# Optimization experiments

Hardware: AMD Instinct MI355X
Metric: run time of the kernel (lower is better)

## Reference

```python
import jax, jax.numpy as jnp
import numpy as np

EMB = 1024
HEADS = 16
HEAD_DIM = EMB // HEADS
BLOCK = 256
N_GLOBAL = 4
WINDOW = 128
ROPE_BASE = 10000.0


def rotate_half(x):
    # interleaved rotate: (-x2_0, x1_0, -x2_1, x1_1, ...), faithful to source
    x1 = x[..., ::2]
    x2 = x[..., 1::2]
    return jnp.stack((-x2, x1), axis=-1).reshape(x.shape)


def setup_inputs() -> dict:
    key = jax.random.key(0)
    k0, k1, k2 = jax.random.split(key, 3)
    B, S = 2, 2048
    x = jax.random.normal(k0, (B, S, EMB), dtype=jnp.float32)
    # Linear weights stored as [in, out]; y = x @ W (bias=False in source)
    w_qkv = jax.random.normal(k1, (EMB, 3 * EMB), dtype=jnp.float32) * (EMB ** -0.5)
    w_out = jax.random.normal(k2, (EMB, EMB), dtype=jnp.float32) * (EMB ** -0.5)
    return {"x": x, "w_qkv": w_qkv, "w_out": w_out}


def _forward(x, w_qkv, w_out):
    B, S, E = x.shape
    H, D = HEADS, HEAD_DIM
    qkv = (x @ w_qkv).reshape(B, S, 3, H, D).transpose(2, 0, 3, 1, 4)  # [3,B,H,S,D]
    q, k, v = qkv[0], qkv[1], qkv[2]

    # Rotary embedding (start_pos = 0, no cache)
    inv_freq = 1.0 / (ROPE_BASE ** (jnp.arange(0, D, 2, dtype=jnp.float32) / D))
    pos = jnp.arange(S, dtype=jnp.float32)
    freqs = jnp.outer(pos, inv_freq)                 # [S, D/2]
    emb = jnp.concatenate([freqs, freqs], axis=-1)   # [S, D]
    cos = jnp.cos(emb)[None, None]                   # [1,1,S,D]
    sin = jnp.sin(emb)[None, None]
    q = q * cos + rotate_half(q) * sin
    k = k * cos + rotate_half(k) * sin

    # Block-local + global-token + sliding-window mask, AND causal (vectorized)
    i = jnp.arange(S)[:, None]
    j = jnp.arange(S)[None, :]
    allowed = (i // BLOCK == j // BLOCK) | (i < N_GLOBAL) | (j < N_GLOBAL) \
              | (jnp.abs(i - j) <= WINDOW)
    allowed = allowed & (j <= i)
    # NOTE: source passes ~mask to F.scaled_dot_product_attention, where a
    # boolean attn_mask with True means "attend". We replicate that exactly.
    attend = ~allowed  # [S, S]

    scale = D ** -0.5
    scores = jnp.einsum("bhsd,bhtd->bhst", q, k) * scale      # [B,H,S,S]
    scores = jnp.where(attend[None, None], scores, jnp.float32(-1e30))
    attn = jax.nn.softmax(scores, axis=-1)
    out = jnp.einsum("bhst,bhtd->bhsd", attn, v)              # [B,H,S,D]
    out = out.transpose(0, 2, 1, 3).reshape(B, S, E)
    return out @ w_out


def reference(x, w_qkv, w_out):
    return _forward(x, w_qkv, w_out)
```

## Files before the change

### kernel.cpp

```cpp
#include <hip/hip_runtime.h>
#include <hip/hip_bf16.h>

#define EMBD   1024
#define NHEAD  16
#define HDIM   64
#define SEQ    2048
#define BATCH  2
#define MROWS  4096
#define NQKV   3072
#define VSTR   2064

using floatx4 = __attribute__((ext_vector_type(4))) float;
using short8  = __attribute__((ext_vector_type(8))) short;

static __device__ __forceinline__ float bf2f(unsigned short u) {
    unsigned int v = ((unsigned int)u) << 16;
    return __uint_as_float(v);
}
static __device__ __forceinline__ unsigned short f2bf(float f) {
    __hip_bfloat16 h = __float2bfloat16(f);
    return *reinterpret_cast<unsigned short*>(&h);
}

__global__ __launch_bounds__(256) void cast_x(
    const float* __restrict__ x, unsigned short* __restrict__ xh,
    unsigned short* __restrict__ xl)
{
    int idx = (blockIdx.x * 256 + threadIdx.x) * 4;
    float4 v = *(const float4*)(x + idx);
    ushort4 h, l;
    h.x = f2bf(v.x); l.x = f2bf(v.x - bf2f(h.x));
    h.y = f2bf(v.y); l.y = f2bf(v.y - bf2f(h.y));
    h.z = f2bf(v.z); l.z = f2bf(v.z - bf2f(h.z));
    h.w = f2bf(v.w); l.w = f2bf(v.w - bf2f(h.w));
    *(ushort4*)(xh + idx) = h;
    *(ushort4*)(xl + idx) = l;
}

__global__ __launch_bounds__(256) void cast_wT(
    const float* __restrict__ w, unsigned short* __restrict__ wT, int N)
{
    __shared__ unsigned short th[64][65];
    const int k0 = blockIdx.y * 64, n0 = blockIdx.x * 64;
    const int t = threadIdx.x;
    const int r = t >> 4, c = (t & 15) * 4;
    for (int rr = r; rr < 64; rr += 16) {
        float4 v = *(const float4*)(w + (size_t)(k0 + rr) * N + n0 + c);
        th[rr][c + 0] = f2bf(v.x);
        th[rr][c + 1] = f2bf(v.y);
        th[rr][c + 2] = f2bf(v.z);
        th[rr][c + 3] = f2bf(v.w);
    }
    __syncthreads();
    for (int rr = r; rr < 64; rr += 16) {
        ushort4 h;
        h.x = th[c + 0][rr]; h.y = th[c + 1][rr];
        h.z = th[c + 2][rr]; h.w = th[c + 3][rr];
        *(ushort4*)(wT + (size_t)(n0 + rr) * 1024 + k0 + c) = h;
    }
}

__global__ __launch_bounds__(256) void gemm_qkv_mfma(
    const unsigned short* __restrict__ xh, const unsigned short* __restrict__ xl,
    const unsigned short* __restrict__ wbT,
    unsigned short* __restrict__ qst, unsigned short* __restrict__ kst,
    unsigned short* __restrict__ vtT)
{
    const int t = threadIdx.x, wave = t >> 6, lane = t & 63;
    const int col = lane & 15, quad = lane >> 4;
    const int n0 = blockIdx.x * 128;
    const int m0 = blockIdx.y * 128;
    const int which = n0 >> 10;
    const int wm = (wave >> 1) * 64, wn = (wave & 1) * 64;

    floatx4 acc[4][4];
    #pragma unroll
    for (int i = 0; i < 4; ++i)
        #pragma unroll
        for (int j = 0; j < 4; ++j) acc[i][j] = (floatx4){0.f, 0.f, 0.f, 0.f};

    const unsigned short* pa_h = xh  + (size_t)(m0 + wm + col) * 1024 + quad * 8;
    const unsigned short* pa_l = xl  + (size_t)(m0 + wm + col) * 1024 + quad * 8;
    const unsigned short* pb   = wbT + (size_t)(n0 + wn + col) * 1024 + quad * 8;

    for (int k0 = 0; k0 < 1024; k0 += 32) {
        short8 bf[4], ah[4], al[4];
        #pragma unroll
        for (int f = 0; f < 4; ++f) bf[f] = *(const short8*)(pb   + f * 16 * 1024 + k0);
        #pragma unroll
        for (int f = 0; f < 4; ++f) ah[f] = *(const short8*)(pa_h + f * 16 * 1024 + k0);
        #pragma unroll
        for (int f = 0; f < 4; ++f) al[f] = *(const short8*)(pa_l + f * 16 * 1024 + k0);

        if (which < 2) {
            #pragma unroll
            for (int fm = 0; fm < 4; ++fm)
                #pragma unroll
                for (int fn = 0; fn < 4; ++fn) {
                    acc[fm][fn] = __builtin_amdgcn_mfma_f32_16x16x32_bf16(
                        bf[fn], ah[fm], acc[fm][fn], 0, 0, 0);
                    acc[fm][fn] = __builtin_amdgcn_mfma_f32_16x16x32_bf16(
                        bf[fn], al[fm], acc[fm][fn], 0, 0, 0);
                }
        } else {
            #pragma unroll
            for (int fm = 0; fm < 4; ++fm)
                #pragma unroll
                for (int fn = 0; fn < 4; ++fn) {
                    acc[fm][fn] = __builtin_amdgcn_mfma_f32_16x16x32_bf16(
                        ah[fm], bf[fn], acc[fm][fn], 0, 0, 0);
                    acc[fm][fn] = __builtin_amdgcn_mfma_f32_16x16x32_bf16(
                        al[fm], bf[fn], acc[fm][fn], 0, 0, 0);
                }
        }
    }

    const float RLOG = 9.210340371976184f / 32.0f;
    if (which < 2) {
        unsigned short* dst = (which == 0) ? qst : kst;
        const float scale = (which == 0) ? 0.125f : 1.0f;
        #pragma unroll
        for (int fm = 0; fm < 4; ++fm) {
            const int s_g = m0 + wm + fm * 16 + col;
            const int b = s_g >> 11, s = s_g & 2047;
            const float sf = (float)s;
            #pragma unroll
            for (int fn = 0; fn < 4; ++fn) {
                const int nl = (n0 & 1023) + wn + fn * 16 + quad * 4;
                const int h = nl >> 6;
                const int d0 = nl & 63;
                floatx4 c = acc[fm][fn];
                float o_[4];
                #pragma unroll
                for (int pp = 0; pp < 2; ++pp) {
                    int de = d0 + pp * 2;
                    float fe = __expf(-(float)(de & 31) * RLOG);
                    float fo = __expf(-(float)((de + 1) & 31) * RLOG);
                    float se, ce, so, co;
                    sincosf(sf * fe, &se, &ce);
                    sincosf(sf * fo, &so, &co);
                    float qe = c[pp * 2], qo = c[pp * 2 + 1];
                    o_[pp * 2]     = (qe * ce - qo * se) * scale;
                    o_[pp * 2 + 1] = (qo * co + qe * so) * scale;
                }
                ushort4 o4;
                o4.x = f2bf(o_[0]); o4.y = f2bf(o_[1]);
                o4.z = f2bf(o_[2]); o4.w = f2bf(o_[3]);
                *(ushort4*)(dst + ((size_t)(b * 16 + h) * 2048 + s) * 64 + d0) = o4;
            }
        }
    } else {
        #pragma unroll
        for (int fm = 0; fm < 4; ++fm) {
            const int m = m0 + wm + fm * 16 + quad * 4;
            const int b = m >> 11, s0 = m & 2047;
            #pragma unroll
            for (int fn = 0; fn < 4; ++fn) {
                const int nl = (n0 & 1023) + wn + fn * 16 + col;
                const int h = nl >> 6;
                const int d = nl & 63;
                floatx4 c = acc[fm][fn];
                ushort4 o4;
                o4.x = f2bf(c[0]); o4.y = f2bf(c[1]);
                o4.z = f2bf(c[2]); o4.w = f2bf(c[3]);
                *(ushort4*)(vtT + (size_t)(b * 16 + h) * 64 * VSTR
                                + (size_t)d * VSTR + s0) = o4;
            }
        }
    }
}

__global__ __launch_bounds__(256) void attn_mfma(
    const unsigned short* __restrict__ qst,
    const unsigned short* __restrict__ kst,
    const unsigned short* __restrict__ vtT,
    unsigned short* __restrict__ attn)
{
    __shared__ __attribute__((aligned(16))) unsigned short p_tile[4][16][40];
    __shared__ float4 redbuf[3][64][5];

    const int tid  = threadIdx.x;
    const int wave = tid >> 6;
    const int lane = tid & 63;
    const int col  = lane & 15;
    const int quad = lane >> 4;

    const int bh   = blockIdx.x >> 7;
    const int row0 = (blockIdx.x & 127) * 16;

    const size_t base  = (size_t)bh * SEQ * HDIM;
    const size_t vbase = (size_t)bh * HDIM * VSTR;

    const unsigned short* qp = qst + base + (size_t)(row0 + col) * HDIM + quad * 8;
    short8 aq0 = *(const short8*)(qp);
    short8 aq1 = *(const short8*)(qp + 32);

    int iR[4], ngR[4], j0R[4];
    #pragma unroll
    for (int r = 0; r < 4; ++r) {
        int i = row0 + quad * 4 + r;
        iR[r] = i;
        ngR[r] = (i + 1 < 4) ? (i + 1) : 4;
        int L = i - 128;
        int bs = (i >> 8) << 8;
        if (bs < L) L = bs;
        if (L < 0) L = 0;
        j0R[r] = (L > 4) ? L : 4;
    }

    floatx4 o0 = {0.f, 0.f, 0.f, 0.f}, o1 = o0, o2 = o0, o3 = o0;
    float lsum[4] = {0.f, 0.f, 0.f, 0.f};

    const int kbeg = wave * (SEQ / 4);

    short8 kf[2][4];
    short8 vf[2][4];

#define LOADK(B, IT) do {                                                         \
        const int kc_ = kbeg + (IT) * 32;                                         \
        const unsigned short* kp_ = kst + base + (size_t)(kc_ + col) * HDIM       \
                                        + quad * 8;                               \
        kf[B][0] = *(const short8*)(kp_);                                         \
        kf[B][1] = *(const short8*)(kp_ + 32);                                    \
        kf[B][2] = *(const short8*)(kp_ + 16 * HDIM);                             \
        kf[B][3] = *(const short8*)(kp_ + 16 * HDIM + 32);                        \
    } while (0)
#define LOADV(B, IT) do {                                                         \
        const int kc_ = kbeg + (IT) * 32;                                         \
        const unsigned short* vp_ = vtT + vbase + (size_t)col * VSTR              \
                                        + kc_ + quad * 8;                         \
        vf[B][0] = *(const short8*)(vp_);                                         \
        vf[B][1] = *(const short8*)(vp_ + 16 * VSTR);                             \
        vf[B][2] = *(const short8*)(vp_ + 32 * VSTR);                             \
        vf[B][3] = *(const short8*)(vp_ + 48 * VSTR);                             \
    } while (0)

    LOADK(0, 0);
    LOADV(0, 0);
    #pragma unroll
    for (int it = 0; it < 16; ++it) {
        const int cur = it & 1;
        if (it < 15) { LOADK(cur ^ 1, it + 1); LOADV(cur ^ 1, it + 1); }

        const int kc0 = kbeg + it * 32;
        #pragma unroll
        for (int h16 = 0; h16 < 2; ++h16) {
            floatx4 s = {0.f, 0.f, 0.f, 0.f};
            s = __builtin_amdgcn_mfma_f32_16x16x32_bf16(aq0, kf[cur][h16 * 2 + 0], s, 0, 0, 0);
            s = __builtin_amdgcn_mfma_f32_16x16x32_bf16(aq1, kf[cur][h16 * 2 + 1], s, 0, 0, 0);
            const int j = kc0 + h16 * 16 + col;
            #pragma unroll
            for (int r = 0; r < 4; ++r) {
                bool excl = (j < ngR[r]) || (j >= j0R[r] && j <= iR[r]);
                float p = excl ? 0.f : __expf(s[r]);
                lsum[r] += p;
                p_tile[wave][quad * 4 + r][h16 * 16 + col] = f2bf(p);
            }
        }
        short8 ap = *(const short8*)&p_tile[wave][col][quad * 8];
        o0 = __builtin_amdgcn_mfma_f32_16x16x32_bf16(ap, vf[cur][0], o0, 0, 0, 0);
        o1 = __builtin_amdgcn_mfma_f32_16x16x32_bf16(ap, vf[cur][1], o1, 0, 0, 0);
        o2 = __builtin_amdgcn_mfma_f32_16x16x32_bf16(ap, vf[cur][2], o2, 0, 0, 0);
        o3 = __builtin_amdgcn_mfma_f32_16x16x32_bf16(ap, vf[cur][3], o3, 0, 0, 0);
    }
#undef LOADK
#undef LOADV

    #pragma unroll
    for (int r = 0; r < 4; ++r) {
        float v = lsum[r];
        v += __shfl_xor(v, 1);
        v += __shfl_xor(v, 2);
        v += __shfl_xor(v, 4);
        v += __shfl_xor(v, 8);
        lsum[r] = v;
    }

    if (wave > 0) {
        redbuf[wave - 1][lane][0] = make_float4(o0[0], o0[1], o0[2], o0[3]);
        redbuf[wave - 1][lane][1] = make_float4(o1[0], o1[1], o1[2], o1[3]);
        redbuf[wave - 1][lane][2] = make_float4(o2[0], o2[1], o2[2], o2[3]);
        redbuf[wave - 1][lane][3] = make_float4(o3[0], o3[1], o3[2], o3[3]);
        redbuf[wave - 1][lane][4] = make_float4(lsum[0], lsum[1], lsum[2], lsum[3]);
    }
    __syncthreads();
    if (wave == 0) {
        #pragma unroll
        for (int w = 0; w < 3; ++w) {
            float4 t0 = redbuf[w][lane][0];
            float4 t1 = redbuf[w][lane][1];
            float4 t2 = redbuf[w][lane][2];
            float4 t3 = redbuf[w][lane][3];
            float4 tl = redbuf[w][lane][4];
            o0[0] += t0.x; o0[1] += t0.y; o0[2] += t0.z; o0[3] += t0.w;
            o1[0] += t1.x; o1[1] += t1.y; o1[2] += t1.z; o1[3] += t1.w;
            o2[0] += t2.x; o2[1] += t2.y; o2[2] += t2.z; o2[3] += t2.w;
            o3[0] += t3.x; o3[1] += t3.y; o3[2] += t3.z; o3[3] += t3.w;
            lsum[0] += tl.x; lsum[1] += tl.y; lsum[2] += tl.z; lsum[3] += tl.w;
        }
        const int b = bh >> 4, h = bh & 15;
        #pragma unroll
        for (int r = 0; r < 4; ++r) {
            float inv = 1.0f / lsum[r];
            unsigned short* orow = attn + ((size_t)(b * SEQ + iR[r])) * EMBD
                                        + h * HDIM + col;
            orow[0]  = f2bf(o0[r] * inv);
            orow[16] = f2bf(o1[r] * inv);
            orow[32] = f2bf(o2[r] * inv);
            orow[48] = f2bf(o3[r] * inv);
        }
    }
}

__global__ __launch_bounds__(256) void gemm_out_mfma(
    const unsigned short* __restrict__ A,
    const unsigned short* __restrict__ woT,
    float* __restrict__ out)
{
    const int t = threadIdx.x, wave = t >> 6, lane = t & 63;
    const int col = lane & 15, quad = lane >> 4;
    const int n0 = blockIdx.x * 128;
    const int m0 = blockIdx.y * 128;
    const int wm = (wave >> 1) * 64, wn = (wave & 1) * 64;

    floatx4 acc[4][4];
    #pragma unroll
    for (int i = 0; i < 4; ++i)
        #pragma unroll
        for (int j = 0; j < 4; ++j) acc[i][j] = (floatx4){0.f, 0.f, 0.f, 0.f};

    const unsigned short* pa = A   + (size_t)(m0 + wm + col) * 1024 + quad * 8;
    const unsigned short* pb = woT + (size_t)(n0 + wn + col) * 1024 + quad * 8;

    for (int k0 = 0; k0 < 1024; k0 += 32) {
        short8 af[4], bf[4];
        #pragma unroll
        for (int f = 0; f < 4; ++f) bf[f] = *(const short8*)(pb + f * 16 * 1024 + k0);
        #pragma unroll
        for (int f = 0; f < 4; ++f) af[f] = *(const short8*)(pa + f * 16 * 1024 + k0);
        #pragma unroll
        for (int fm = 0; fm < 4; ++fm)
            #pragma unroll
            for (int fn = 0; fn < 4; ++fn)
                acc[fm][fn] = __builtin_amdgcn_mfma_f32_16x16x32_bf16(
                    af[fm], bf[fn], acc[fm][fn], 0, 0, 0);
    }

    #pragma unroll
    for (int fm = 0; fm < 4; ++fm) {
        const int m = m0 + wm + fm * 16 + quad * 4;
        #pragma unroll
        for (int fn = 0; fn < 4; ++fn) {
            const int n = n0 + wn + fn * 16 + col;
            floatx4 c = acc[fm][fn];
            out[(size_t)(m + 0) * 1024 + n] = c[0];
            out[(size_t)(m + 1) * 1024 + n] = c[1];
            out[(size_t)(m + 2) * 1024 + n] = c[2];
            out[(size_t)(m + 3) * 1024 + n] = c[3];
        }
    }
}

extern "C" void kernel_launch(void* const* d_in, const int* in_sizes, int n_in,
                              void* d_out, int out_size, void* d_ws, size_t ws_size,
                              hipStream_t stream) {
    const float* x     = (const float*)d_in[0];
    const float* w_qkv = (const float*)d_in[1];
    const float* w_out = (const float*)d_in[2];
    float* out = (float*)d_out;

    unsigned short* ws16 = (unsigned short*)d_ws;
    unsigned short* xh  = ws16;
    unsigned short* xl  = ws16 +  4194304;
    unsigned short* wbT = ws16 +  8388608;
    unsigned short* woT = ws16 + 11534336;
    unsigned short* qst = ws16 + 12582912;
    unsigned short* kst = ws16 + 16777216;
    unsigned short* vtT = ws16 + 20971520;
    unsigned short* aws = ws16 + 25198592;

    dim3 blk(256);
    cast_x<<<dim3(4096), blk, 0, stream>>>(x, xh, xl);
    cast_wT<<<dim3(48, 16), blk, 0, stream>>>(w_qkv, wbT, NQKV);
    cast_wT<<<dim3(16, 16), blk, 0, stream>>>(w_out, woT, EMBD);

    gemm_qkv_mfma<<<dim3(NQKV / 128, MROWS / 128), blk, 0, stream>>>(
        xh, xl, wbT, qst, kst, vtT);

    attn_mfma<<<dim3(32 * 128), blk, 0, stream>>>(qst, kst, vtT, aws);

    gemm_out_mfma<<<dim3(EMBD / 128, MROWS / 128), blk, 0, stream>>>(aws, woT, out);
}
```

Measured before the change: 429.1 us.

## Process two 16-row query tiles per attention block to reuse K/V fragments

Each attention workgroup now handles 32 query rows, two 16-row MFMA tiles, instead of 16, so every K and V fragment loaded from global memory feeds twice as many MFMAs. The grid is halved to match, and the shared-memory buffers and accumulators are doubled. A sched_barrier is added after the prefetch loads to keep them ahead of the compute. The cost is roughly double the accumulator registers and LDS per block, which may lower occupancy, and fewer blocks in the grid.

Result: faster. 367.0 us (-14.5%).

```diff
diff --git a/kernel.cpp b/kernel.cpp
--- a/kernel.cpp
+++ b/kernel.cpp
@@ -176,8 +176,8 @@
     const unsigned short* __restrict__ vtT,
     unsigned short* __restrict__ attn)
 {
-    __shared__ __attribute__((aligned(16))) unsigned short p_tile[4][16][40];
-    __shared__ float4 redbuf[3][64][5];
+    __shared__ __attribute__((aligned(16))) unsigned short p_tile[2][4][16][40];
+    __shared__ float4 redbuf[3][64][2][5];
 
     const int tid  = threadIdx.x;
     const int wave = tid >> 6;
@@ -185,31 +185,45 @@
     const int col  = lane & 15;
     const int quad = lane >> 4;
 
-    const int bh   = blockIdx.x >> 7;
-    const int row0 = (blockIdx.x & 127) * 16;
+    const int bh   = blockIdx.x >> 6;
+    const int row0 = (blockIdx.x & 63) * 32;
 
     const size_t base  = (size_t)bh * SEQ * HDIM;
     const size_t vbase = (size_t)bh * HDIM * VSTR;
 
-    const unsigned short* qp = qst + base + (size_t)(row0 + col) * HDIM + quad * 8;
-    short8 aq0 = *(const short8*)(qp);
-    short8 aq1 = *(const short8*)(qp + 32);
-
-    int iR[4], ngR[4], j0R[4];
-    #pragma unroll
-    for (int r = 0; r < 4; ++r) {
-        int i = row0 + quad * 4 + r;
-        iR[r] = i;
-        ngR[r] = (i + 1 < 4) ? (i + 1) : 4;
-        int L = i - 128;
-        int bs = (i >> 8) << 8;
-        if (bs < L) L = bs;
-        if (L < 0) L = 0;
-        j0R[r] = (L > 4) ? L : 4;
-    }
-
-    floatx4 o0 = {0.f, 0.f, 0.f, 0.f}, o1 = o0, o2 = o0, o3 = o0;
-    float lsum[4] = {0.f, 0.f, 0.f, 0.f};
+    short8 aq[2][2];
+    #pragma unroll
+    for (int tt = 0; tt < 2; ++tt) {
+        const unsigned short* qp = qst + base
+            + (size_t)(row0 + tt * 16 + col) * HDIM + quad * 8;
+        aq[tt][0] = *(const short8*)(qp);
+        aq[tt][1] = *(const short8*)(qp + 32);
+    }
+
+    int iR[2][4], ngR[2][4], j0R[2][4];
+    #pragma unroll
+    for (int tt = 0; tt < 2; ++tt)
+        #pragma unroll
+        for (int r = 0; r < 4; ++r) {
+            int i = row0 + tt * 16 + quad * 4 + r;
+            iR[tt][r] = i;
+            ngR[tt][r] = (i + 1 < 4) ? (i + 1) : 4;
+            int L = i - 128;
+            int bs = (i >> 8) << 8;
+            if (bs < L) L = bs;
+            if (L < 0) L = 0;
+            j0R[tt][r] = (L > 4) ? L : 4;
+        }
+
+    floatx4 o[2][4];
+    float lsum[2][4];
+    #pragma unroll
+    for (int tt = 0; tt < 2; ++tt)
+        #pragma unroll
+        for (int r = 0; r < 4; ++r) {
+            o[tt][r] = (floatx4){0.f, 0.f, 0.f, 0.f};
+            lsum[tt][r] = 0.f;
+        }
 
     const int kbeg = wave * (SEQ / 4);
 
@@ -241,74 +255,92 @@
     for (int it = 0; it < 16; ++it) {
         const int cur = it & 1;
         if (it < 15) { LOADK(cur ^ 1, it + 1); LOADV(cur ^ 1, it + 1); }
+        __builtin_amdgcn_sched_barrier(0);
 
         const int kc0 = kbeg + it * 32;
         #pragma unroll
         for (int h16 = 0; h16 < 2; ++h16) {
-            floatx4 s = {0.f, 0.f, 0.f, 0.f};
-            s = __builtin_amdgcn_mfma_f32_16x16x32_bf16(aq0, kf[cur][h16 * 2 + 0], s, 0, 0, 0);
-            s = __builtin_amdgcn_mfma_f32_16x16x32_bf16(aq1, kf[cur][h16 * 2 + 1], s, 0, 0, 0);
             const int j = kc0 + h16 * 16 + col;
             #pragma unroll
-            for (int r = 0; r < 4; ++r) {
-                bool excl = (j < ngR[r]) || (j >= j0R[r] && j <= iR[r]);
-                float p = excl ? 0.f : __expf(s[r]);
-                lsum[r] += p;
-                p_tile[wave][quad * 4 + r][h16 * 16 + col] = f2bf(p);
+            for (int tt = 0; tt < 2; ++tt) {
+                floatx4 s = {0.f, 0.f, 0.f, 0.f};
+                s = __builtin_amdgcn_mfma_f32_16x16x32_bf16(
+                        aq[tt][0], kf[cur][h16 * 2 + 0], s, 0, 0, 0);
+                s = __builtin_amdgcn_mfma_f32_16x16x32_bf16(
+                        aq[tt][1], kf[cur][h16 * 2 + 1], s, 0, 0, 0);
+                #pragma unroll
+                for (int r = 0; r < 4; ++r) {
+                    bool excl = (j < ngR[tt][r]) || (j >= j0R[tt][r] && j <= iR[tt][r]);
+                    float p = excl ? 0.f : __expf(s[r]);
+                    lsum[tt][r] += p;
+                    p_tile[tt][wave][quad * 4 + r][h16 * 16 + col] = f2bf(p);
+                }
             }
         }
-        short8 ap = *(const short8*)&p_tile[wave][col][quad * 8];
-        o0 = __builtin_amdgcn_mfma_f32_16x16x32_bf16(ap, vf[cur][0], o0, 0, 0, 0);
-        o1 = __builtin_amdgcn_mfma_f32_16x16x32_bf16(ap, vf[cur][1], o1, 0, 0, 0);
-        o2 = __builtin_amdgcn_mfma_f32_16x16x32_bf16(ap, vf[cur][2], o2, 0, 0, 0);
-        o3 = __builtin_amdgcn_mfma_f32_16x16x32_bf16(ap, vf[cur][3], o3, 0, 0, 0);
+        #pragma unroll
+        for (int tt = 0; tt < 2; ++tt) {
+            short8 ap = *(const short8*)&p_tile[tt][wave][col][quad * 8];
+            o[tt][0] = __builtin_amdgcn_mfma_f32_16x16x32_bf16(ap, vf[cur][0], o[tt][0], 0, 0, 0);
+            o[tt][1] = __builtin_amdgcn_mfma_f32_16x16x32_bf16(ap, vf[cur][1], o[tt][1], 0, 0, 0);
+            o[tt][2] = __builtin_amdgcn_mfma_f32_16x16x32_bf16(ap, vf[cur][2], o[tt][2], 0, 0, 0);
+            o[tt][3] = __builtin_amdgcn_mfma_f32_16x16x32_bf16(ap, vf[cur][3], o[tt][3], 0, 0, 0);
+        }
     }
 #undef LOADK
 #undef LOADV
 
     #pragma unroll
-    for (int r = 0; r < 4; ++r) {
-        float v = lsum[r];
-        v += __shfl_xor(v, 1);
-        v += __shfl_xor(v, 2);
-        v += __shfl_xor(v, 4);
-        v += __shfl_xor(v, 8);
-        lsum[r] = v;
-    }
+    for (int tt = 0; tt < 2; ++tt)
+        #pragma unroll
+        for (int r = 0; r < 4; ++r) {
+            float v = lsum[tt][r];
+            v += __shfl_xor(v, 1);
+            v += __shfl_xor(v, 2);
+            v += __shfl_xor(v, 4);
+            v += __shfl_xor(v, 8);
+            lsum[tt][r] = v;
+        }
 
     if (wave > 0) {
-        redbuf[wave - 1][lane][0] = make_float4(o0[0], o0[1], o0[2], o0[3]);
-        redbuf[wave - 1][lane][1] = make_float4(o1[0], o1[1], o1[2], o1[3]);
-        redbuf[wave - 1][lane][2] = make_float4(o2[0], o2[1], o2[2], o2[3]);
-        redbuf[wave - 1][lane][3] = make_float4(o3[0], o3[1], o3[2], o3[3]);
-        redbuf[wave - 1][lane][4] = make_float4(lsum[0], lsum[1], lsum[2], lsum[3]);
+        #pragma unroll
+        for (int tt = 0; tt < 2; ++tt) {
+            redbuf[wave - 1][lane][tt][0] = make_float4(o[tt][0][0], o[tt][0][1], o[tt][0][2], o[tt][0][3]);
+            redbuf[wave - 1][lane][tt][1] = make_float4(o[tt][1][0], o[tt][1][1], o[tt][1][2], o[tt][1][3]);
+            redbuf[wave - 1][lane][tt][2] = make_float4(o[tt][2][0], o[tt][2][1], o[tt][2][2], o[tt][2][3]);
+            redbuf[wave - 1][lane][tt][3] = make_float4(o[tt][3][0], o[tt][3][1], o[tt][3][2], o[tt][3][3]);
+            redbuf[wave - 1][lane][tt][4] = make_float4(lsum[tt][0], lsum[tt][1], lsum[tt][2], lsum[tt][3]);
+        }
     }
     __syncthreads();
     if (wave == 0) {
         #pragma unroll
-        for (int w = 0; w < 3; ++w) {
-            float4 t0 = redbuf[w][lane][0];
-            float4 t1 = redbuf[w][lane][1];
-            float4 t2 = redbuf[w][lane][2];
-            float4 t3 = redbuf[w][lane][3];
-            float4 tl = redbuf[w][lane][4];
-            o0[0] += t0.x; o0[1] += t0.y; o0[2] += t0.z; o0[3] += t0.w;
-            o1[0] += t1.x; o1[1] += t1.y; o1[2] += t1.z; o1[3] += t1.w;
-            o2[0] += t2.x; o2[1] += t2.y; o2[2] += t2.z; o2[3] += t2.w;
-            o3[0] += t3.x; o3[1] += t3.y; o3[2] += t3.z; o3[3] += t3.w;
-            lsum[0] += tl.x; lsum[1] += tl.y; lsum[2] += tl.z; lsum[3] += tl.w;
-        }
+        for (int w = 0; w < 3; ++w)
+            #pragma unroll
+            for (int tt = 0; tt < 2; ++tt) {
+                float4 t0 = redbuf[w][lane][tt][0];
+                float4 t1 = redbuf[w][lane][tt][1];
+                float4 t2 = redbuf[w][lane][tt][2];
+                float4 t3 = redbuf[w][lane][tt][3];
+                float4 tl = redbuf[w][lane][tt][4];
+                o[tt][0][0] += t0.x; o[tt][0][1] += t0.y; o[tt][0][2] += t0.z; o[tt][0][3] += t0.w;
+                o[tt][1][0] += t1.x; o[tt][1][1] += t1.y; o[tt][1][2] += t1.z; o[tt][1][3] += t1.w;
+                o[tt][2][0] += t2.x; o[tt][2][1] += t2.y; o[tt][2][2] += t2.z; o[tt][2][3] += t2.w;
+                o[tt][3][0] += t3.x; o[tt][3][1] += t3.y; o[tt][3][2] += t3.z; o[tt][3][3] += t3.w;
+                lsum[tt][0] += tl.x; lsum[tt][1] += tl.y; lsum[tt][2] += tl.z; lsum[tt][3] += tl.w;
+            }
         const int b = bh >> 4, h = bh & 15;
         #pragma unroll
-        for (int r = 0; r < 4; ++r) {
-            float inv = 1.0f / lsum[r];
-            unsigned short* orow = attn + ((size_t)(b * SEQ + iR[r])) * EMBD
-                                        + h * HDIM + col;
-            orow[0]  = f2bf(o0[r] * inv);
-            orow[16] = f2bf(o1[r] * inv);
-            orow[32] = f2bf(o2[r] * inv);
-            orow[48] = f2bf(o3[r] * inv);
-        }
+        for (int tt = 0; tt < 2; ++tt)
+            #pragma unroll
+            for (int r = 0; r < 4; ++r) {
+                float inv = 1.0f / lsum[tt][r];
+                unsigned short* orow = attn + ((size_t)(b * SEQ + iR[tt][r])) * EMBD
+                                            + h * HDIM + col;
+                orow[0]  = f2bf(o[tt][0][r] * inv);
+                orow[16] = f2bf(o[tt][1][r] * inv);
+                orow[32] = f2bf(o[tt][2][r] * inv);
+                orow[48] = f2bf(o[tt][3][r] * inv);
+            }
     }
 }
 
@@ -387,7 +419,7 @@
     gemm_qkv_mfma<<<dim3(NQKV / 128, MROWS / 128), blk, 0, stream>>>(
         xh, xl, wbT, qst, kst, vtT);
 
-    attn_mfma<<<dim3(32 * 128), blk, 0, stream>>>(qst, kst, vtT, aws);
+    attn_mfma<<<dim3(32 * 64), blk, 0, stream>>>(qst, kst, vtT, aws);
 
     gemm_out_mfma<<<dim3(EMBD / 128, MROWS / 128), blk, 0, stream>>>(aws, woT, out);
 }
```
